# Kernel tuning notes

Measured on AMD Instinct MI355X. Metric: run time of the kernel, lower is better.

Reference implementation:

```python
import jax, jax.numpy as jnp
import numpy as np
from jax.scipy.special import logsumexp

D = 256; H = 8; A = D // H
B_CONST = 0.9; P_MAX = 50000.0; P_MIN = 1e-4; TANH_RATE = 0.005; EPS = 1e-10
SCALE = 1.0 / np.sqrt(D)


def setup_inputs() -> dict:
    key = jax.random.key(0)
    ks = jax.random.split(key, 5)
    B, S = 2, 512
    context = jax.random.normal(ks[0], (B, S, D), dtype=jnp.float32)
    W_Q = jax.random.normal(ks[1], (D, D), dtype=jnp.float32) * (1.0 / np.sqrt(D))
    W_KV = jax.random.normal(ks[2], (2 * D, D), dtype=jnp.float32) * (1.0 / np.sqrt(D))
    W_out = jax.random.normal(ks[3], (D, D), dtype=jnp.float32) * (1.0 / np.sqrt(D))
    p_param = jax.random.normal(ks[4], (D,), dtype=jnp.float32) * 0.02
    return {"context": context, "W_Q": W_Q, "W_KV": W_KV, "W_out": W_out, "p_param": p_param}


def reference(context, W_Q, W_KV, W_out, p_param):
    B, S, _ = context.shape
    # projections (nn.Linear: x @ W.T)
    q = context @ W_Q.T                          # [B,S,D]
    kv = context @ W_KV.T                        # [B,S,2D]
    k, v = kv[..., :D], kv[..., D:]
    # scaled p: p_max*tanh(tanh_rate*p)+1, then replace exact zeros with p_min
    p = P_MAX * jnp.tanh(TANH_RATE * p_param) + 1.0
    p = p + (p == 0).astype(p.dtype) * P_MIN
    # minmax-normalize v over the key/sequence axis into [b, 1]
    v_max = jnp.max(v, axis=-2, keepdims=True)   # [B,1,D]
    v_min = jnp.min(v, axis=-2, keepdims=True)
    v = (1.0 - B_CONST) * (v - v_min) / (v_max - v_min + EPS) + B_CONST
    z = p * jnp.log(v)                           # [B,S,D]
    # split heads
    qh = q.reshape(B, S, H, A).transpose(0, 2, 1, 3)          # [B,H,S,A]
    kh = k.reshape(B, S, H, A).transpose(0, 2, 1, 3)          # [B,H,S,A]
    zh = z.reshape(B, S, H, A).transpose(0, 2, 1, 3)[:, :, None]  # [B,H,1,K,A]
    dot = jnp.einsum('bhqa,bhka->bhqk', qh, kh)
    w = jax.nn.log_softmax(dot * SCALE, axis=-1)              # [B,H,Q,K]
    # log-domain power mean: logsumexp over keys of log-weights + p*log(v)
    mean = logsumexp(w[..., None] + zh, axis=-2)              # [B,H,Q,A]
    mean = mean.transpose(0, 2, 1, 3).reshape(B, S, D)
    e = jnp.exp(mean / p)
    # invert v minmax normalization
    e = (e - B_CONST) * (v_max - v_min + EPS) / (1.0 - B_CONST) + v_min
    return e @ W_out.T
```

## Files before the change

kernel.cpp:

```cpp
#include <hip/hip_runtime.h>
#include <math.h>

constexpr float BCONST      = 0.9f;
constexpr float ONE_MINUS_B = 0.1f;
constexpr float EPSF        = 1e-10f;
constexpr float SCALEF      = 0.0625f;

#define OFF_QKV    0
#define OFF_VP     786432
#define OFF_EW     1048576
#define OFF_PMIN   1310720
#define OFF_PMAX   1318912
#define OFF_VMIN   1327104
#define OFF_VRANGE 1327616
#define OFF_P      1328128

#define KB4(buf, row, col4) \
  (&(buf)[((row) << 5) | ((((col4) >> 2) ^ (((row) >> 2) & 7)) << 2)])

template<int TM, int TN, int RM, int RN, bool MM>
__global__ __launch_bounds__(256) void gemm_t(
    const float* __restrict__ A, const float* __restrict__ B0,
    const float* __restrict__ B1, int nsplit,
    float* __restrict__ C, int ldc, int K, int lda,
    float* __restrict__ pminP, float* __restrict__ pmaxP) {
  constexpr int LDT = 36;
  constexpr int CG  = TN / RN;
  constexpr int NA  = TM * 32 / 1024;
  constexpr int NB  = TN * 32 / 1024;
  __shared__ float As[TM][LDT];
  __shared__ float Bs[TN][LDT];
  const int i0 = blockIdx.x * TM;
  const int j0 = blockIdx.y * TN;
  const float* Bsrc = (j0 < nsplit) ? (B0 + (size_t)j0 * K)
                                    : (B1 + (size_t)(j0 - nsplit) * K);
  const int t  = threadIdx.x;
  const int lr = t >> 3;
  const int lc = (t & 7) << 2;
  const int tx = t % CG, ty = t / CG;

  float4 pa[NA], pb[NB];
#pragma unroll
  for (int u = 0; u < NA; ++u)
    pa[u] = *(const float4*)(A + (size_t)(i0 + lr + 32 * u) * lda + lc);
#pragma unroll
  for (int u = 0; u < NB; ++u)
    pb[u] = *(const float4*)(Bsrc + (size_t)(lr + 32 * u) * K + lc);

  float acc[RM][RN] = {};
  for (int k0 = 0; k0 < K; k0 += 32) {
    __syncthreads();
#pragma unroll
    for (int u = 0; u < NA; ++u) *(float4*)&As[lr + 32 * u][lc] = pa[u];
#pragma unroll
    for (int u = 0; u < NB; ++u) *(float4*)&Bs[lr + 32 * u][lc] = pb[u];
    __syncthreads();
    if (k0 + 32 < K) {
#pragma unroll
      for (int u = 0; u < NA; ++u)
        pa[u] = *(const float4*)(A + (size_t)(i0 + lr + 32 * u) * lda + k0 + 32 + lc);
#pragma unroll
      for (int u = 0; u < NB; ++u)
        pb[u] = *(const float4*)(Bsrc + (size_t)(lr + 32 * u) * K + k0 + 32 + lc);
    }
#pragma unroll
    for (int kk = 0; kk < 32; kk += 4) {
      float4 af[RM], bf[RN];
#pragma unroll
      for (int r = 0; r < RM; ++r) af[r] = *(const float4*)&As[ty * RM + r][kk];
#pragma unroll
      for (int c = 0; c < RN; ++c) bf[c] = *(const float4*)&Bs[tx + CG * c][kk];
#pragma unroll
      for (int r = 0; r < RM; ++r)
#pragma unroll
        for (int c = 0; c < RN; ++c)
          acc[r][c] += af[r].x * bf[c].x + af[r].y * bf[c].y +
                       af[r].z * bf[c].z + af[r].w * bf[c].w;
    }
  }
#pragma unroll
  for (int r = 0; r < RM; ++r)
#pragma unroll
    for (int c = 0; c < RN; ++c)
      C[(size_t)(i0 + ty * RM + r) * ldc + j0 + tx + CG * c] = acc[r][c];

  if (MM && j0 >= 512) {
    __syncthreads();
    float* mnb = &As[0][0];
    float* mxb = &Bs[0][0];
#pragma unroll
    for (int c = 0; c < RN; ++c) {
      float mn = acc[0][c], mx = acc[0][c];
#pragma unroll
      for (int r = 1; r < RM; ++r) {
        mn = fminf(mn, acc[r][c]);
        mx = fmaxf(mx, acc[r][c]);
      }
      mnb[(tx + CG * c) * 17 + ty] = mn;
      mxb[(tx + CG * c) * 17 + ty] = mx;
    }
    __syncthreads();
    if (t < TN) {
      float mn = mnb[t * 17], mx = mxb[t * 17];
#pragma unroll
      for (int i = 1; i < 16; ++i) {
        mn = fminf(mn, mnb[t * 17 + i]);
        mx = fmaxf(mx, mxb[t * 17 + i]);
      }
      const int bx = i0 >> 5;
      pminP[bx * 256 + (j0 - 512) + t] = mn;
      pmaxP[bx * 256 + (j0 - 512) + t] = mx;
    }
  }
}

__global__ __launch_bounds__(256) void vpk(
    const float* __restrict__ qkv, const float* __restrict__ pminP,
    const float* __restrict__ pmaxP, const float* __restrict__ p_param,
    float* __restrict__ vp, float* __restrict__ vminw,
    float* __restrict__ vrangew, float* __restrict__ pw) {
  const int blk = blockIdx.x;
  const int b = blk >> 9, s = blk & 511;
  const int d = threadIdx.x;
  float mn = pminP[(b * 16) * 256 + d];
  float mx = pmaxP[(b * 16) * 256 + d];
#pragma unroll
  for (int c = 1; c < 16; ++c) {
    mn = fminf(mn, pminP[(b * 16 + c) * 256 + d]);
    mx = fmaxf(mx, pmaxP[(b * 16 + c) * 256 + d]);
  }
  float p = 50000.0f * tanhf(0.005f * p_param[d]) + 1.0f;
  if (p == 0.0f) p = 0.0001f;
  const float range = mx - mn + EPSF;
  const float v  = qkv[((size_t)(b * 512 + s)) * 768 + 512 + d];
  const float vn = (ONE_MINUS_B * (v - mn)) / range + BCONST;
  vp[(size_t)blk * 256 + d] = expm1f(p * logf(vn));
  if (s == 0) { vminw[b * 256 + d] = mn; vrangew[b * 256 + d] = range; }
  if (blk == 0) pw[d] = p;
}

__global__ __launch_bounds__(512) void attn_k(
    const float* __restrict__ qkv, const float* __restrict__ vp,
    const float* __restrict__ pw, const float* __restrict__ vminw,
    const float* __restrict__ vrangew, float* __restrict__ ew) {
  __shared__ float qs[32][36];
  __shared__ float sc[32 * 516];
  __shared__ float kb[512 * 32];
  __shared__ float red[32];
  const int bh  = blockIdx.y;
  const int b   = bh >> 3, h = bh & 7;
  const int q0g = blockIdx.x * 32;
  const int t   = threadIdx.x;
  const int srow = t >> 3, scol4 = (t & 7) << 2;

  if (t < 256) {
    const int q = t >> 3, c4 = (t & 7) << 2;
    float4 qv = *(const float4*)(qkv + ((size_t)(b * 512 + q0g + q)) * 768 + h * 32 + c4);
    qv.x *= SCALEF; qv.y *= SCALEF; qv.z *= SCALEF; qv.w *= SCALEF;
    *(float4*)&qs[q][c4] = qv;
  }
#pragma unroll 8
  for (int u = 0; u < 8; ++u) {
    const int r = srow + 64 * u;
    float4 v = *(const float4*)(qkv + ((size_t)(b * 512 + r)) * 768 + 256 + h * 32 + scol4);
    *(float4*)KB4(kb, r, scol4) = v;
  }
  __syncthreads();

  {
    const int qgw = t >> 6;
    const int kg  = t & 63;
    float s8[4][8] = {};
#pragma unroll 2
    for (int kk = 0; kk < 32; kk += 4) {
      float4 qf[4], kf1[4], kf2[4];
#pragma unroll
      for (int r = 0; r < 4; ++r) qf[r] = *(const float4*)&qs[qgw + 8 * r][kk];
#pragma unroll
      for (int c = 0; c < 4; ++c) {
        kf1[c] = *(const float4*)KB4(kb, kg * 4 + c, kk);
        kf2[c] = *(const float4*)KB4(kb, 256 + kg * 4 + c, kk);
      }
#pragma unroll
      for (int r = 0; r < 4; ++r)
#pragma unroll
        for (int c = 0; c < 4; ++c) {
          s8[r][c]     += qf[r].x * kf1[c].x + qf[r].y * kf1[c].y +
                          qf[r].z * kf1[c].z + qf[r].w * kf1[c].w;
          s8[r][4 + c] += qf[r].x * kf2[c].x + qf[r].y * kf2[c].y +
                          qf[r].z * kf2[c].z + qf[r].w * kf2[c].w;
        }
    }
    float rs[4];
#pragma unroll
    for (int r = 0; r < 4; ++r) {
      float s = 0.f;
#pragma unroll
      for (int c = 0; c < 8; ++c) {
        s8[r][c] = __expf(s8[r][c]);
        s += s8[r][c];
      }
      rs[r] = s;
    }
#pragma unroll
    for (int m = 1; m < 64; m <<= 1)
#pragma unroll
      for (int r = 0; r < 4; ++r) rs[r] += __shfl_xor(rs[r], m);
    if ((t & 63) == 0)
#pragma unroll
      for (int r = 0; r < 4; ++r) red[qgw + 8 * r] = rs[r];
#pragma unroll
    for (int r = 0; r < 4; ++r) {
      const int rq = qgw + 8 * r;
      *(float4*)&sc[rq * 516 + kg * 4] =
          make_float4(s8[r][0], s8[r][1], s8[r][2], s8[r][3]);
      *(float4*)&sc[rq * 516 + 256 + kg * 4] =
          make_float4(s8[r][4], s8[r][5], s8[r][6], s8[r][7]);
    }
  }
  __syncthreads();

#pragma unroll 8
  for (int u = 0; u < 8; ++u) {
    const int r = srow + 64 * u;
    float4 v = *(const float4*)(vp + ((size_t)(b * 512 + r)) * 256 + h * 32 + scol4);
    *(float4*)KB4(kb, r, scol4) = v;
  }
  __syncthreads();

  const int ag = t & 7;
  const int qg = (t >> 3) & 7;
  const int ks = t >> 6;
  float a3[4][4] = {};
#pragma unroll 2
  for (int g = 0; g < 16; ++g) {
    const int kbase = ks * 64 + g * 4;
    float4 sq[4], vf[4];
#pragma unroll
    for (int r = 0; r < 4; ++r)
      sq[r] = *(const float4*)&sc[(qg + 8 * r) * 516 + kbase];
#pragma unroll
    for (int c = 0; c < 4; ++c)
      vf[c] = *(const float4*)KB4(kb, kbase + c, ag * 4);
#pragma unroll
    for (int r = 0; r < 4; ++r) {
      a3[r][0] += sq[r].x * vf[0].x + sq[r].y * vf[1].x + sq[r].z * vf[2].x + sq[r].w * vf[3].x;
      a3[r][1] += sq[r].x * vf[0].y + sq[r].y * vf[1].y + sq[r].z * vf[2].y + sq[r].w * vf[3].y;
      a3[r][2] += sq[r].x * vf[0].z + sq[r].y * vf[1].z + sq[r].z * vf[2].z + sq[r].w * vf[3].z;
      a3[r][3] += sq[r].x * vf[0].w + sq[r].y * vf[1].w + sq[r].z * vf[2].w + sq[r].w * vf[3].w;
    }
  }
  __syncthreads();
  float* part = &kb[0];
  {
#pragma unroll
    for (int r = 0; r < 4; ++r)
#pragma unroll
      for (int c = 0; c < 4; ++c)
        part[ks * 1152 + (qg + 8 * r) * 36 + ag * 4 + c] = a3[r][c];
  }
  __syncthreads();

  if (t < 256) {
    const int q = t >> 3, a0 = (t & 7) << 2;
    const int d0 = h * 32 + a0;
    const float invT = 1.0f / red[q];
    float4 s0 = *(const float4*)&part[q * 36 + a0];
#pragma unroll
    for (int w = 1; w < 8; ++w) {
      float4 sw = *(const float4*)&part[w * 1152 + q * 36 + a0];
      s0.x += sw.x; s0.y += sw.y; s0.z += sw.z; s0.w += sw.w;
    }
    const float4 pp = *(const float4*)(pw + d0);
    const float4 vr = *(const float4*)(vrangew + b * 256 + d0);
    const float4 vm = *(const float4*)(vminw + b * 256 + d0);
    float4 o;
    o.x = (expf(log1pf(s0.x * invT) / pp.x) - BCONST) * vr.x / ONE_MINUS_B + vm.x;
    o.y = (expf(log1pf(s0.y * invT) / pp.y) - BCONST) * vr.y / ONE_MINUS_B + vm.y;
    o.z = (expf(log1pf(s0.z * invT) / pp.z) - BCONST) * vr.z / ONE_MINUS_B + vm.z;
    o.w = (expf(log1pf(s0.w * invT) / pp.w) - BCONST) * vr.w / ONE_MINUS_B + vm.w;
    *(float4*)(ew + ((size_t)(b * 512 + q0g + q)) * 256 + d0) = o;
  }
}

extern "C" void kernel_launch(void* const* d_in, const int* in_sizes, int n_in,
                              void* d_out, int out_size, void* d_ws, size_t ws_size,
                              hipStream_t stream) {
  const float* ctx  = (const float*)d_in[0];
  const float* WQ   = (const float*)d_in[1];
  const float* WKV  = (const float*)d_in[2];
  const float* WOUT = (const float*)d_in[3];
  const float* PP   = (const float*)d_in[4];
  float* ws      = (float*)d_ws;
  float* qkv     = ws + OFF_QKV;
  float* vp      = ws + OFF_VP;
  float* ew      = ws + OFF_EW;
  float* pminP   = ws + OFF_PMIN;
  float* pmaxP   = ws + OFF_PMAX;
  float* vminw   = ws + OFF_VMIN;
  float* vrangew = ws + OFF_VRANGE;
  float* pw      = ws + OFF_P;
  float* out     = (float*)d_out;

  gemm_t<32, 32, 2, 2, true><<<dim3(32, 24), 256, 0, stream>>>(
      ctx, WQ, WKV, 256, qkv, 768, 256, 256, pminP, pmaxP);
  vpk<<<1024, 256, 0, stream>>>(qkv, pminP, pmaxP, PP, vp, vminw, vrangew, pw);
  attn_k<<<dim3(16, 16), 512, 0, stream>>>(qkv, vp, pw, vminw, vrangew, ew);
  gemm_t<32, 32, 2, 2, false><<<dim3(32, 8), 256, 0, stream>>>(
      ew, WOUT, WOUT, 1 << 30, out, 256, 256, 256, nullptr, nullptr);
}
```

Baseline: 99.70 us.

## Double threads per block in attention and output GEMM kernels

```diff
diff --git a/kernel.cpp b/kernel.cpp
--- a/kernel.cpp
+++ b/kernel.cpp
@@ -18,16 +18,14 @@
 #define KB4(buf, row, col4) \
   (&(buf)[((row) << 5) | ((((col4) >> 2) ^ (((row) >> 2) & 7)) << 2)])
 
-template<int TM, int TN, int RM, int RN, bool MM>
-__global__ __launch_bounds__(256) void gemm_t(
+template<int NT, int TM, int TN, int RM, int RN, bool MM>
+__global__ __launch_bounds__(NT) void gemm_t(
     const float* __restrict__ A, const float* __restrict__ B0,
     const float* __restrict__ B1, int nsplit,
     float* __restrict__ C, int ldc, int K, int lda,
     float* __restrict__ pminP, float* __restrict__ pmaxP) {
   constexpr int LDT = 36;
   constexpr int CG  = TN / RN;
-  constexpr int NA  = TM * 32 / 1024;
-  constexpr int NB  = TN * 32 / 1024;
   __shared__ float As[TM][LDT];
   __shared__ float Bs[TN][LDT];
   const int i0 = blockIdx.x * TM;
@@ -39,29 +37,19 @@
   const int lc = (t & 7) << 2;
   const int tx = t % CG, ty = t / CG;
 
-  float4 pa[NA], pb[NB];
-#pragma unroll
-  for (int u = 0; u < NA; ++u)
-    pa[u] = *(const float4*)(A + (size_t)(i0 + lr + 32 * u) * lda + lc);
-#pragma unroll
-  for (int u = 0; u < NB; ++u)
-    pb[u] = *(const float4*)(Bsrc + (size_t)(lr + 32 * u) * K + lc);
+  float4 pa, pb;
+  if (lr < TM) pa = *(const float4*)(A + (size_t)(i0 + lr) * lda + lc);
+  if (lr < TN) pb = *(const float4*)(Bsrc + (size_t)lr * K + lc);
 
   float acc[RM][RN] = {};
   for (int k0 = 0; k0 < K; k0 += 32) {
     __syncthreads();
-#pragma unroll
-    for (int u = 0; u < NA; ++u) *(float4*)&As[lr + 32 * u][lc] = pa[u];
-#pragma unroll
-    for (int u = 0; u < NB; ++u) *(float4*)&Bs[lr + 32 * u][lc] = pb[u];
+    if (lr < TM) *(float4*)&As[lr][lc] = pa;
+    if (lr < TN) *(float4*)&Bs[lr][lc] = pb;
     __syncthreads();
     if (k0 + 32 < K) {
-#pragma unroll
-      for (int u = 0; u < NA; ++u)
-        pa[u] = *(const float4*)(A + (size_t)(i0 + lr + 32 * u) * lda + k0 + 32 + lc);
-#pragma unroll
-      for (int u = 0; u < NB; ++u)
-        pb[u] = *(const float4*)(Bsrc + (size_t)(lr + 32 * u) * K + k0 + 32 + lc);
+      if (lr < TM) pa = *(const float4*)(A + (size_t)(i0 + lr) * lda + k0 + 32 + lc);
+      if (lr < TN) pb = *(const float4*)(Bsrc + (size_t)lr * K + k0 + 32 + lc);
     }
 #pragma unroll
     for (int kk = 0; kk < 32; kk += 4) {
@@ -139,14 +127,16 @@
   if (blk == 0) pw[d] = p;
 }
 
-__global__ __launch_bounds__(512) void attn_k(
+__global__ __launch_bounds__(1024) void attn_k(
     const float* __restrict__ qkv, const float* __restrict__ vp,
     const float* __restrict__ pw, const float* __restrict__ vminw,
     const float* __restrict__ vrangew, float* __restrict__ ew) {
-  __shared__ float qs[32][36];
-  __shared__ float sc[32 * 516];
-  __shared__ float kb[512 * 32];
-  __shared__ float red[32];
+  __shared__ float S[34080];
+  float* qs  = S;
+  float* sc  = S + 1152;
+  float* kb  = S + 17664;
+  float* red = S + 34048;
+  float* part = S;
   const int bh  = blockIdx.y;
   const int b   = bh >> 3, h = bh & 7;
   const int q0g = blockIdx.x * 32;
@@ -157,32 +147,32 @@
     const int q = t >> 3, c4 = (t & 7) << 2;
     float4 qv = *(const float4*)(qkv + ((size_t)(b * 512 + q0g + q)) * 768 + h * 32 + c4);
     qv.x *= SCALEF; qv.y *= SCALEF; qv.z *= SCALEF; qv.w *= SCALEF;
-    *(float4*)&qs[q][c4] = qv;
-  }
-#pragma unroll 8
-  for (int u = 0; u < 8; ++u) {
-    const int r = srow + 64 * u;
+    *(float4*)&qs[q * 36 + c4] = qv;
+  }
+#pragma unroll
+  for (int u = 0; u < 4; ++u) {
+    const int r = srow + 128 * u;
     float4 v = *(const float4*)(qkv + ((size_t)(b * 512 + r)) * 768 + 256 + h * 32 + scol4);
     *(float4*)KB4(kb, r, scol4) = v;
   }
   __syncthreads();
 
   {
-    const int qgw = t >> 6;
-    const int kg  = t & 63;
-    float s8[4][8] = {};
+    const int w  = t >> 6;
+    const int kg = t & 63;
+    float s8[2][8] = {};
 #pragma unroll 2
     for (int kk = 0; kk < 32; kk += 4) {
-      float4 qf[4], kf1[4], kf2[4];
-#pragma unroll
-      for (int r = 0; r < 4; ++r) qf[r] = *(const float4*)&qs[qgw + 8 * r][kk];
+      float4 qf[2], kf1[4], kf2[4];
+#pragma unroll
+      for (int r = 0; r < 2; ++r) qf[r] = *(const float4*)&qs[(w + 16 * r) * 36 + kk];
 #pragma unroll
       for (int c = 0; c < 4; ++c) {
         kf1[c] = *(const float4*)KB4(kb, kg * 4 + c, kk);
         kf2[c] = *(const float4*)KB4(kb, 256 + kg * 4 + c, kk);
       }
 #pragma unroll
-      for (int r = 0; r < 4; ++r)
+      for (int r = 0; r < 2; ++r)
 #pragma unroll
         for (int c = 0; c < 4; ++c) {
           s8[r][c]     += qf[r].x * kf1[c].x + qf[r].y * kf1[c].y +
@@ -191,9 +181,9 @@
                           qf[r].z * kf2[c].z + qf[r].w * kf2[c].w;
         }
     }
-    float rs[4];
-#pragma unroll
-    for (int r = 0; r < 4; ++r) {
+    float rs[2];
+#pragma unroll
+    for (int r = 0; r < 2; ++r) {
       float s = 0.f;
 #pragma unroll
       for (int c = 0; c < 8; ++c) {
@@ -205,13 +195,13 @@
 #pragma unroll
     for (int m = 1; m < 64; m <<= 1)
 #pragma unroll
-      for (int r = 0; r < 4; ++r) rs[r] += __shfl_xor(rs[r], m);
+      for (int r = 0; r < 2; ++r) rs[r] += __shfl_xor(rs[r], m);
     if ((t & 63) == 0)
 #pragma unroll
-      for (int r = 0; r < 4; ++r) red[qgw + 8 * r] = rs[r];
-#pragma unroll
-    for (int r = 0; r < 4; ++r) {
-      const int rq = qgw + 8 * r;
+      for (int r = 0; r < 2; ++r) red[w + 16 * r] = rs[r];
+#pragma unroll
+    for (int r = 0; r < 2; ++r) {
+      const int rq = w + 16 * r;
       *(float4*)&sc[rq * 516 + kg * 4] =
           make_float4(s8[r][0], s8[r][1], s8[r][2], s8[r][3]);
       *(float4*)&sc[rq * 516 + 256 + kg * 4] =
@@ -220,21 +210,22 @@
   }
   __syncthreads();
 
-#pragma unroll 8
-  for (int u = 0; u < 8; ++u) {
-    const int r = srow + 64 * u;
+#pragma unroll
+  for (int u = 0; u < 4; ++u) {
+    const int r = srow + 128 * u;
     float4 v = *(const float4*)(vp + ((size_t)(b * 512 + r)) * 256 + h * 32 + scol4);
     *(float4*)KB4(kb, r, scol4) = v;
   }
   __syncthreads();
 
-  const int ag = t & 7;
-  const int qg = (t >> 3) & 7;
+  const int lane = t & 63;
+  const int ag = lane & 7;
+  const int qg = lane >> 3;
   const int ks = t >> 6;
   float a3[4][4] = {};
-#pragma unroll 2
-  for (int g = 0; g < 16; ++g) {
-    const int kbase = ks * 64 + g * 4;
+#pragma unroll
+  for (int g = 0; g < 8; ++g) {
+    const int kbase = ks * 32 + g * 4;
     float4 sq[4], vf[4];
 #pragma unroll
     for (int r = 0; r < 4; ++r)
@@ -251,14 +242,11 @@
     }
   }
   __syncthreads();
-  float* part = &kb[0];
-  {
-#pragma unroll
-    for (int r = 0; r < 4; ++r)
-#pragma unroll
-      for (int c = 0; c < 4; ++c)
-        part[ks * 1152 + (qg + 8 * r) * 36 + ag * 4 + c] = a3[r][c];
-  }
+#pragma unroll
+  for (int r = 0; r < 4; ++r)
+#pragma unroll
+    for (int c = 0; c < 4; ++c)
+      part[ks * 1152 + (qg + 8 * r) * 36 + ag * 4 + c] = a3[r][c];
   __syncthreads();
 
   if (t < 256) {
@@ -267,7 +255,7 @@
     const float invT = 1.0f / red[q];
     float4 s0 = *(const float4*)&part[q * 36 + a0];
 #pragma unroll
-    for (int w = 1; w < 8; ++w) {
+    for (int w = 1; w < 16; ++w) {
       float4 sw = *(const float4*)&part[w * 1152 + q * 36 + a0];
       s0.x += sw.x; s0.y += sw.y; s0.z += sw.z; s0.w += sw.w;
     }
@@ -302,10 +290,10 @@
   float* pw      = ws + OFF_P;
   float* out     = (float*)d_out;
 
-  gemm_t<32, 32, 2, 2, true><<<dim3(32, 24), 256, 0, stream>>>(
+  gemm_t<256, 32, 32, 2, 2, true><<<dim3(32, 24), 256, 0, stream>>>(
       ctx, WQ, WKV, 256, qkv, 768, 256, 256, pminP, pmaxP);
   vpk<<<1024, 256, 0, stream>>>(qkv, pminP, pmaxP, PP, vp, vminw, vrangew, pw);
-  attn_k<<<dim3(16, 16), 512, 0, stream>>>(qkv, vp, pw, vminw, vrangew, ew);
-  gemm_t<32, 32, 2, 2, false><<<dim3(32, 8), 256, 0, stream>>>(
+  attn_k<<<dim3(16, 16), 1024, 0, stream>>>(qkv, vp, pw, vminw, vrangew, ew);
+  gemm_t<512, 32, 32, 2, 1, false><<<dim3(32, 8), 512, 0, stream>>>(
       ew, WOUT, WOUT, 1 << 30, out, 256, 256, 256, nullptr, nullptr);
 }
```

Result: slower. 148.7 us (+49.2%).
